# Kernel optimization log

Measured on AMD Instinct MI355X. Metric: run time of the kernel, lower is better.

## Reference

```python
import jax, jax.numpy as jnp
import numpy as np

DIM = 1024
NHEADS = 16
HEAD_DIM = DIM // NHEADS
SCALE = HEAD_DIM ** -0.5
B, N = 4, 2048


def setup_inputs() -> dict:
    key = jax.random.key(0)
    ks = jax.random.split(key, 11)
    s = 1.0 / np.sqrt(DIM)
    inp = {
        "query": jax.random.normal(ks[0], (B, N, DIM), jnp.float32),
        "key": jax.random.normal(ks[1], (B, N, DIM), jnp.float32),
        "value": jax.random.normal(ks[2], (B, N, DIM), jnp.float32),
        "Wq": jax.random.normal(ks[3], (DIM, DIM), jnp.float32) * s,
        "bq": jnp.zeros((DIM,), jnp.float32),
        "Wk": jax.random.normal(ks[4], (DIM, DIM), jnp.float32) * s,
        "bk": jnp.zeros((DIM,), jnp.float32),
        "Wv": jax.random.normal(ks[5], (DIM, DIM), jnp.float32) * s,
        "bv": jnp.zeros((DIM,), jnp.float32),
        "Wo": jax.random.normal(ks[6], (DIM, DIM), jnp.float32) * s,
        "bo": jnp.zeros((DIM,), jnp.float32),
    }
    return inp


def reference(query, key, value, Wq, bq, Wk, bk, Wv, bv, Wo, bo):
    b, n, c = query.shape
    # linear projections (torch Linear: x @ W.T + b)
    q = query @ Wq.T + bq
    k = key @ Wk.T + bk
    v = value @ Wv.T + bv
    # 'b n (h d) -> (b h) n d'
    def split_heads(t):
        return t.reshape(b, -1, NHEADS, HEAD_DIM).transpose(0, 2, 1, 3).reshape(b * NHEADS, -1, HEAD_DIM)
    q, k, v = split_heads(q), split_heads(k), split_heads(v)
    attn = jax.nn.softmax(jnp.einsum('bnd,bmd->bnm', q, k) * SCALE, axis=-1)
    # faithful to original: raw reshape [(b h), n, d] -> [b, n, c] (no head transpose back)
    x = jnp.einsum('bnm,bmd->bnd', attn, v).reshape(b, n, c)
    x = x @ Wo.T + bo
    return x
```

## Files before the change

### kernel.cpp

```cpp
#include <hip/hip_runtime.h>
#include <cstdint>
#include <cstddef>

#define NHEADS 16
#define HD 64
#define SEQ 2048
#define BATCH 4
#define DIMSZ 1024
#define MR (BATCH * SEQ)

typedef __attribute__((ext_vector_type(8))) short short8;
typedef __attribute__((ext_vector_type(4))) float f32x4;

typedef __attribute__((address_space(1))) const unsigned int as1_u32;
typedef __attribute__((address_space(3))) unsigned int as3_u32;

__device__ __forceinline__ unsigned short f2bf(float x) {
  union { float f; unsigned int u; } v; v.f = x;
  unsigned int r = v.u + 0x7FFFu + ((v.u >> 16) & 1u);
  return (unsigned short)(r >> 16);
}

__device__ __forceinline__ f32x4 mfma16(short8 a, short8 b, f32x4 c) {
  return __builtin_amdgcn_mfma_f32_16x16x32_bf16(a, b, c, 0, 0, 0);
}

__device__ __forceinline__ void gload_lds16(const void* g, void* l) {
  __builtin_amdgcn_global_load_lds((as1_u32*)g, (as3_u32*)l, 16, 0, 0);
}

__device__ __forceinline__ int swzfn(int r) { return ((r ^ (r >> 3)) & 7) << 4; }

struct Cvt7 {
  const float* s[7];
  unsigned short* d[7];
  int n4[7];
};

__global__ __launch_bounds__(256) void cvt7_k(Cvt7 a) {
  const int t = blockIdx.y;
  const float4* s = (const float4*)a.s[t];
  ushort4* d = (ushort4*)a.d[t];
  const int n4 = a.n4[t];
  for (int i = blockIdx.x * 256 + threadIdx.x; i < n4; i += gridDim.x * 256) {
    float4 f = s[i];
    ushort4 u;
    u.x = f2bf(f.x); u.y = f2bf(f.y); u.z = f2bf(f.z); u.w = f2bf(f.w);
    d[i] = u;
  }
}

struct GemmArgs {
  const unsigned short* A[3];
  const unsigned short* Bt[3];
  const float* bias[3];
  unsigned short* Cb[3];
  float* Cf[3];
  float scale[3];
  int vt[3];
};

template <bool BF16OUT>
__global__ __launch_bounds__(256) void gemm_bt_k(GemmArgs g) {
  const int z = blockIdx.z;
  const unsigned short* __restrict__ A = g.A[z];
  const unsigned short* __restrict__ Bt = g.Bt[z];
  const float* __restrict__ bias = g.bias[z];

  __shared__ unsigned short As[128 * 32];
  __shared__ unsigned short Bs[128 * 32];

  const int tid = threadIdx.x;
  const int lane = tid & 63;
  const int wave = tid >> 6;
  const int bm = blockIdx.x * 128;
  const int bn = blockIdx.y * 128;
  const int wm = (wave >> 1) * 64;
  const int wn = (wave & 1) * 64;

  const int srow = wave * 16 + (lane >> 2);
  const int scol = (lane & 3) * 8;
  const unsigned short* a_src = A + (size_t)(bm + srow) * DIMSZ + scol;
  const unsigned short* b_src = Bt + (size_t)(bn + srow) * DIMSZ + scol;
  char* a_dst = (char*)As + (size_t)(wave * 16) * 64;
  char* b_dst = (char*)Bs + (size_t)(wave * 16) * 64;

  const int fr = lane & 15;
  const int fk = (lane >> 4) * 8;

  f32x4 acc[4][4];
#pragma unroll
  for (int m = 0; m < 4; m++)
#pragma unroll
    for (int n = 0; n < 4; n++) acc[m][n] = (f32x4){0.f, 0.f, 0.f, 0.f};

  for (int k0 = 0; k0 < DIMSZ; k0 += 32) {
    __syncthreads();
    gload_lds16(a_src + k0, a_dst);
    gload_lds16(a_src + (size_t)64 * DIMSZ + k0, a_dst + 64 * 64);
    gload_lds16(b_src + k0, b_dst);
    gload_lds16(b_src + (size_t)64 * DIMSZ + k0, b_dst + 64 * 64);
    __syncthreads();

    short8 af[4], bfr[4];
#pragma unroll
    for (int m = 0; m < 4; m++) af[m] = *(const short8*)&As[(wm + m * 16 + fr) * 32 + fk];
#pragma unroll
    for (int n = 0; n < 4; n++) bfr[n] = *(const short8*)&Bs[(wn + n * 16 + fr) * 32 + fk];
#pragma unroll
    for (int m = 0; m < 4; m++)
#pragma unroll
      for (int n = 0; n < 4; n++) acc[m][n] = mfma16(af[m], bfr[n], acc[m][n]);
  }

  const int r4 = (lane >> 4) * 4;
  const float sc = g.scale[z];
  if (g.vt[z]) {
    unsigned short* vtp = g.Cb[z];
#pragma unroll
    for (int n = 0; n < 4; n++) {
      const int c = bn + wn + n * 16 + fr;
      const float bv = bias[c];
#pragma unroll
      for (int m = 0; m < 4; m++) {
        const int rr = bm + wm + m * 16 + r4;
        ushort4 u;
        u.x = f2bf((acc[m][n][0] + bv) * sc);
        u.y = f2bf((acc[m][n][1] + bv) * sc);
        u.z = f2bf((acc[m][n][2] + bv) * sc);
        u.w = f2bf((acc[m][n][3] + bv) * sc);
        const size_t idx =
            ((size_t)((rr >> 11) * NHEADS + (c >> 6)) * HD + (c & 63)) * SEQ + (rr & (SEQ - 1));
        *(ushort4*)&vtp[idx] = u;
      }
    }
  } else {
#pragma unroll
    for (int n = 0; n < 4; n++) {
      const int c = bn + wn + n * 16 + fr;
      const float bv = bias[c];
#pragma unroll
      for (int m = 0; m < 4; m++) {
#pragma unroll
        for (int j = 0; j < 4; j++) {
          const int r = bm + wm + m * 16 + r4 + j;
          const float val = (acc[m][n][j] + bv) * sc;
          if (BF16OUT)
            g.Cb[z][(size_t)r * DIMSZ + c] = f2bf(val);
          else
            g.Cf[z][(size_t)r * DIMSZ + c] = val;
        }
      }
    }
  }
}

__global__ __launch_bounds__(256) void attn_k(const unsigned short* __restrict__ q,
                                              const unsigned short* __restrict__ k,
                                              const unsigned short* __restrict__ vt,
                                              unsigned short* __restrict__ o) {
  const int tid = threadIdx.x;
  const int lane = tid & 63;
  const int wave = tid >> 6;
  const int bh = blockIdx.y;
  const int b = bh >> 4;
  const int h = bh & 15;
  const int q0 = blockIdx.x * 64;

  __shared__ unsigned short Ks[2][64 * 64];
  __shared__ unsigned short Vs[2][64 * 64];

  const int fr = lane & 15;
  const int g4 = lane >> 4;
  const int fkb = g4 * 16;

  const size_t qrow = (size_t)b * SEQ + q0 + wave * 16 + fr;
  const unsigned short* qp = q + qrow * DIMSZ + h * HD + g4 * 8;
  const short8 qa0 = *(const short8*)(qp);
  const short8 qa1 = *(const short8*)(qp + 32);

  float m_run = -1e30f, l_run = 0.f;
  f32x4 oacc[4];
#pragma unroll
  for (int n = 0; n < 4; n++) oacc[n] = (f32x4){0.f, 0.f, 0.f, 0.f};

  const size_t kvbase = (size_t)b * SEQ * DIMSZ + h * HD;
  const size_t vtbase = (size_t)bh * HD * SEQ;
  const int klrow = lane >> 3;
  const int kcb = (lane & 7) * 16;

  auto stage = [&](int t, int buf) {
    const int kv0 = t * 64;
#pragma unroll
    for (int i = 0; i < 2; i++) {
      const int row = wave * 8 + i * 32 + klrow;
      const int scol = (kcb ^ swzfn(row)) >> 1;
      gload_lds16(k + kvbase + (size_t)(kv0 + row) * DIMSZ + scol,
                  (char*)Ks[buf] + (wave * 8 + i * 32) * 128);
      gload_lds16(vt + vtbase + (size_t)row * SEQ + kv0 + scol,
                  (char*)Vs[buf] + (wave * 8 + i * 32) * 128);
    }
  };

  stage(0, 0);
  __syncthreads();
  int cur = 0;

  for (int t = 0; t < SEQ / 64; ++t) {
    if (t + 1 < SEQ / 64) stage(t + 1, cur ^ 1);

    const char* Kc = (const char*)Ks[cur];
    const char* Vc = (const char*)Vs[cur];

    f32x4 s[4];
#pragma unroll
    for (int n = 0; n < 4; n++) {
      const int row = fr + 16 * n;
      const int swz = swzfn(row);
      const short8 kb0 = *(const short8*)(Kc + ((row * 128 + fkb) ^ swz));
      const short8 kb1 = *(const short8*)(Kc + ((row * 128 + 64 + fkb) ^ swz));
      f32x4 tacc = (f32x4){0.f, 0.f, 0.f, 0.f};
      tacc = mfma16(kb0, qa0, tacc);
      tacc = mfma16(kb1, qa1, tacc);
      s[n] = tacc;
    }

    float pm = -1e30f;
#pragma unroll
    for (int n = 0; n < 4; n++)
#pragma unroll
      for (int jj = 0; jj < 4; jj++) pm = fmaxf(pm, s[n][jj]);
    pm = fmaxf(pm, __shfl_xor(pm, 16));
    pm = fmaxf(pm, __shfl_xor(pm, 32));
    const float mn = fmaxf(m_run, pm);
    const float sf = __expf(m_run - mn);
    m_run = mn;

    float pe[4][4];
    float rs = 0.f;
#pragma unroll
    for (int n = 0; n < 4; n++)
#pragma unroll
      for (int jj = 0; jj < 4; jj++) {
        const float p = __expf(s[n][jj] - mn);
        pe[n][jj] = p;
        rs += p;
      }
    rs += __shfl_xor(rs, 16);
    rs += __shfl_xor(rs, 32);
    l_run = l_run * sf + rs;

    unsigned P32[4][2];
#pragma unroll
    for (int n = 0; n < 4; n++) {
      P32[n][0] = (unsigned)f2bf(pe[n][0]) | ((unsigned)f2bf(pe[n][1]) << 16);
      P32[n][1] = (unsigned)f2bf(pe[n][2]) | ((unsigned)f2bf(pe[n][3]) << 16);
    }

    const int myn = g4 & 1;
    const int srcA = fr + 16 * ((g4 & 1) * 2 + (g4 >> 1));
    const int srcB = fr + 16 * ((g4 & 1) * 2 + ((g4 >> 1) ^ 1));
    const unsigned xA0 = myn ? P32[1][0] : P32[0][0];
    const unsigned xA1 = myn ? P32[1][1] : P32[0][1];
    const unsigned xB0 = myn ? P32[0][0] : P32[1][0];
    const unsigned xB1 = myn ? P32[0][1] : P32[1][1];
    const unsigned xC0 = myn ? P32[3][0] : P32[2][0];
    const unsigned xC1 = myn ? P32[3][1] : P32[2][1];
    const unsigned xD0 = myn ? P32[2][0] : P32[3][0];
    const unsigned xD1 = myn ? P32[2][1] : P32[3][1];
    const unsigned A0 = (unsigned)__shfl((int)xA0, srcA);
    const unsigned A1 = (unsigned)__shfl((int)xA1, srcA);
    const unsigned B0 = (unsigned)__shfl((int)xB0, srcB);
    const unsigned B1 = (unsigned)__shfl((int)xB1, srcB);
    const unsigned C0 = (unsigned)__shfl((int)xC0, srcA);
    const unsigned C1 = (unsigned)__shfl((int)xC1, srcA);
    const unsigned D0 = (unsigned)__shfl((int)xD0, srcB);
    const unsigned D1 = (unsigned)__shfl((int)xD1, srcB);

    const bool lohalf = (g4 < 2);
    union { unsigned u[4]; short8 v; } pa0, pa1;
    pa0.u[0] = lohalf ? A0 : B0;
    pa0.u[1] = lohalf ? A1 : B1;
    pa0.u[2] = lohalf ? B0 : A0;
    pa0.u[3] = lohalf ? B1 : A1;
    pa1.u[0] = lohalf ? C0 : D0;
    pa1.u[1] = lohalf ? C1 : D1;
    pa1.u[2] = lohalf ? D0 : C0;
    pa1.u[3] = lohalf ? D1 : C1;

    float sfr[4];
#pragma unroll
    for (int jj = 0; jj < 4; jj++) sfr[jj] = __shfl(sf, 20 * g4 + jj);
#pragma unroll
    for (int n = 0; n < 4; n++)
#pragma unroll
      for (int jj = 0; jj < 4; jj++) oacc[n][jj] *= sfr[jj];

#pragma unroll
    for (int n = 0; n < 4; n++) {
      const int row = fr + 16 * n;
      const int swz = swzfn(row);
      const short8 vb0 = *(const short8*)(Vc + ((row * 128 + fkb) ^ swz));
      const short8 vb1 = *(const short8*)(Vc + ((row * 128 + 64 + fkb) ^ swz));
      oacc[n] = mfma16(pa0.v, vb0, oacc[n]);
      oacc[n] = mfma16(pa1.v, vb1, oacc[n]);
    }

    __syncthreads();
    cur ^= 1;
  }

  float lr[4];
#pragma unroll
  for (int jj = 0; jj < 4; jj++) lr[jj] = __shfl(l_run, 20 * g4 + jj);
#pragma unroll
  for (int n = 0; n < 4; n++)
#pragma unroll
    for (int jj = 0; jj < 4; jj++) {
      const int row = q0 + wave * 16 + 4 * g4 + jj;
      const float val = oacc[n][jj] / lr[jj];
      o[((size_t)bh * SEQ + row) * HD + fr + 16 * n] = f2bf(val);
    }
}

extern "C" void kernel_launch(void* const* d_in, const int* in_sizes, int n_in,
                              void* d_out, int out_size, void* d_ws, size_t ws_size,
                              hipStream_t stream) {
  (void)in_sizes; (void)n_in; (void)out_size; (void)ws_size;
  const float* query = (const float*)d_in[0];
  const float* key_i = (const float*)d_in[1];
  const float* value = (const float*)d_in[2];
  const float* Wq = (const float*)d_in[3];
  const float* bq = (const float*)d_in[4];
  const float* Wk = (const float*)d_in[5];
  const float* bk = (const float*)d_in[6];
  const float* Wv = (const float*)d_in[7];
  const float* bv = (const float*)d_in[8];
  const float* Wo = (const float*)d_in[9];
  const float* bo = (const float*)d_in[10];
  float* out = (float*)d_out;

  char* ws = (char*)d_ws;
  size_t off = 0;
  auto alloc = [&](size_t bytes) -> char* {
    char* p = ws + off;
    off += (bytes + 255) & ~(size_t)255;
    return p;
  };
  const size_t big = (size_t)MR * DIMSZ * 2;
  const size_t wsz = (size_t)DIMSZ * DIMSZ * 2;
  unsigned short* xq = (unsigned short*)alloc(big);
  unsigned short* xk = (unsigned short*)alloc(big);
  unsigned short* xv = (unsigned short*)alloc(big);
  unsigned short* wqb = (unsigned short*)alloc(wsz);
  unsigned short* wkb = (unsigned short*)alloc(wsz);
  unsigned short* wvb = (unsigned short*)alloc(wsz);
  unsigned short* wob = (unsigned short*)alloc(wsz);
  unsigned short* qb = (unsigned short*)alloc(big);
  unsigned short* kb = (unsigned short*)alloc(big);
  unsigned short* vtb = (unsigned short*)alloc(big);
  unsigned short* ob = xq;

  Cvt7 ca;
  ca.s[0] = query; ca.d[0] = xq; ca.n4[0] = MR * DIMSZ / 4;
  ca.s[1] = key_i; ca.d[1] = xk; ca.n4[1] = MR * DIMSZ / 4;
  ca.s[2] = value; ca.d[2] = xv; ca.n4[2] = MR * DIMSZ / 4;
  ca.s[3] = Wq;    ca.d[3] = wqb; ca.n4[3] = DIMSZ * DIMSZ / 4;
  ca.s[4] = Wk;    ca.d[4] = wkb; ca.n4[4] = DIMSZ * DIMSZ / 4;
  ca.s[5] = Wv;    ca.d[5] = wvb; ca.n4[5] = DIMSZ * DIMSZ / 4;
  ca.s[6] = Wo;    ca.d[6] = wob; ca.n4[6] = DIMSZ * DIMSZ / 4;
  cvt7_k<<<dim3(1024, 7), 256, 0, stream>>>(ca);

  GemmArgs gp;
  gp.A[0] = xq; gp.A[1] = xk; gp.A[2] = xv;
  gp.Bt[0] = wqb; gp.Bt[1] = wkb; gp.Bt[2] = wvb;
  gp.bias[0] = bq; gp.bias[1] = bk; gp.bias[2] = bv;
  gp.Cb[0] = qb; gp.Cb[1] = kb; gp.Cb[2] = vtb;
  gp.Cf[0] = nullptr; gp.Cf[1] = nullptr; gp.Cf[2] = nullptr;
  gp.scale[0] = 0.125f; gp.scale[1] = 1.f; gp.scale[2] = 1.f;
  gp.vt[0] = 0; gp.vt[1] = 0; gp.vt[2] = 1;
  gemm_bt_k<true><<<dim3(MR / 128, DIMSZ / 128, 3), 256, 0, stream>>>(gp);

  attn_k<<<dim3(SEQ / 64, BATCH * NHEADS), 256, 0, stream>>>(qb, kb, vtb, ob);

  GemmArgs go;
  go.A[0] = ob; go.A[1] = ob; go.A[2] = ob;
  go.Bt[0] = wob; go.Bt[1] = wob; go.Bt[2] = wob;
  go.bias[0] = bo; go.bias[1] = bo; go.bias[2] = bo;
  go.Cb[0] = nullptr; go.Cb[1] = nullptr; go.Cb[2] = nullptr;
  go.Cf[0] = out; go.Cf[1] = out; go.Cf[2] = out;
  go.scale[0] = 1.f; go.scale[1] = 1.f; go.scale[2] = 1.f;
  go.vt[0] = 0; go.vt[1] = 0; go.vt[2] = 0;
  gemm_bt_k<false><<<dim3(MR / 128, DIMSZ / 128, 1), 256, 0, stream>>>(go);
}
```

Baseline: 424.1 us.

## Use 8-wave attention blocks sharing K/V tiles and drop P shuffles

Each attention block now covers 128 queries with 8 waves instead of 64 with 4, so every K/V tile staged in LDS serves twice as many query rows and each wave issues one async load per tile rather than two. The cross-lane shuffle that rearranged P into the MFMA A-operand layout is removed; V is instead read from LDS as two 4-element halves whose offsets match P's native layout. The row-sum reduction across lanes moves out of the loop to the epilogue, and swizzled LDS offsets are precomputed before the loop. In exchange there are half as many blocks, more registers per thread for the offset tables, and more 8-byte LDS reads.

Measured after the change: 391.9 us. 7.6% less time.

```diff
diff --git a/kernel.cpp b/kernel.cpp
--- a/kernel.cpp
+++ b/kernel.cpp
@@ -10,6 +10,7 @@
 #define MR (BATCH * SEQ)
 
 typedef __attribute__((ext_vector_type(8))) short short8;
+typedef __attribute__((ext_vector_type(4))) short short4v;
 typedef __attribute__((ext_vector_type(4))) float f32x4;
 
 typedef __attribute__((address_space(1))) const unsigned int as1_u32;
@@ -155,7 +156,7 @@
   }
 }
 
-__global__ __launch_bounds__(256) void attn_k(const unsigned short* __restrict__ q,
+__global__ __launch_bounds__(512) void attn_k(const unsigned short* __restrict__ q,
                                               const unsigned short* __restrict__ k,
                                               const unsigned short* __restrict__ vt,
                                               unsigned short* __restrict__ o) {
@@ -165,7 +166,7 @@
   const int bh = blockIdx.y;
   const int b = bh >> 4;
   const int h = bh & 15;
-  const int q0 = blockIdx.x * 64;
+  const int q0 = blockIdx.x * 128;
 
   __shared__ unsigned short Ks[2][64 * 64];
   __shared__ unsigned short Vs[2][64 * 64];
@@ -184,22 +185,31 @@
 #pragma unroll
   for (int n = 0; n < 4; n++) oacc[n] = (f32x4){0.f, 0.f, 0.f, 0.f};
 
-  const size_t kvbase = (size_t)b * SEQ * DIMSZ + h * HD;
-  const size_t vtbase = (size_t)bh * HD * SEQ;
+  int koff[4][2];
+  int voff[4][4];
+#pragma unroll
+  for (int n = 0; n < 4; n++) {
+    const int row = fr + 16 * n;
+    const int swz = swzfn(row);
+    koff[n][0] = (row * 128 + fkb) ^ swz;
+    koff[n][1] = (row * 128 + 64 + fkb) ^ swz;
+#pragma unroll
+    for (int c = 0; c < 4; c++) voff[n][c] = (row * 128 + (c * 32 + 8 * g4)) ^ swz;
+  }
+
   const int klrow = lane >> 3;
   const int kcb = (lane & 7) * 16;
+  const int srow = wave * 8 + klrow;
+  const int scol = (kcb ^ swzfn(srow)) >> 1;
+  const unsigned short* ksrc =
+      k + (size_t)b * SEQ * DIMSZ + h * HD + (size_t)srow * DIMSZ + scol;
+  const unsigned short* vsrc =
+      vt + (size_t)bh * HD * SEQ + (size_t)srow * SEQ + scol;
 
   auto stage = [&](int t, int buf) {
-    const int kv0 = t * 64;
-#pragma unroll
-    for (int i = 0; i < 2; i++) {
-      const int row = wave * 8 + i * 32 + klrow;
-      const int scol = (kcb ^ swzfn(row)) >> 1;
-      gload_lds16(k + kvbase + (size_t)(kv0 + row) * DIMSZ + scol,
-                  (char*)Ks[buf] + (wave * 8 + i * 32) * 128);
-      gload_lds16(vt + vtbase + (size_t)row * SEQ + kv0 + scol,
-                  (char*)Vs[buf] + (wave * 8 + i * 32) * 128);
-    }
+    const size_t kv0 = (size_t)t * 64;
+    gload_lds16(ksrc + kv0 * DIMSZ, (char*)Ks[buf] + wave * 1024);
+    gload_lds16(vsrc + kv0, (char*)Vs[buf] + wave * 1024);
   };
 
   stage(0, 0);
@@ -215,10 +225,8 @@
     f32x4 s[4];
 #pragma unroll
     for (int n = 0; n < 4; n++) {
-      const int row = fr + 16 * n;
-      const int swz = swzfn(row);
-      const short8 kb0 = *(const short8*)(Kc + ((row * 128 + fkb) ^ swz));
-      const short8 kb1 = *(const short8*)(Kc + ((row * 128 + 64 + fkb) ^ swz));
+      const short8 kb0 = *(const short8*)(Kc + koff[n][0]);
+      const short8 kb1 = *(const short8*)(Kc + koff[n][1]);
       f32x4 tacc = (f32x4){0.f, 0.f, 0.f, 0.f};
       tacc = mfma16(kb0, qa0, tacc);
       tacc = mfma16(kb1, qa1, tacc);
@@ -236,90 +244,58 @@
     const float sf = __expf(m_run - mn);
     m_run = mn;
 
-    float pe[4][4];
+    unsigned pu[4][2];
     float rs = 0.f;
 #pragma unroll
+    for (int n = 0; n < 4; n++) {
+      const float p0 = __expf(s[n][0] - mn);
+      const float p1 = __expf(s[n][1] - mn);
+      const float p2 = __expf(s[n][2] - mn);
+      const float p3 = __expf(s[n][3] - mn);
+      rs += (p0 + p1) + (p2 + p3);
+      pu[n][0] = (unsigned)f2bf(p0) | ((unsigned)f2bf(p1) << 16);
+      pu[n][1] = (unsigned)f2bf(p2) | ((unsigned)f2bf(p3) << 16);
+    }
+    l_run = l_run * sf + rs;
+
+    float sfr[4];
+#pragma unroll
+    for (int jj = 0; jj < 4; jj++) sfr[jj] = __shfl(sf, 20 * g4 + jj);
+#pragma unroll
     for (int n = 0; n < 4; n++)
 #pragma unroll
-      for (int jj = 0; jj < 4; jj++) {
-        const float p = __expf(s[n][jj] - mn);
-        pe[n][jj] = p;
-        rs += p;
-      }
-    rs += __shfl_xor(rs, 16);
-    rs += __shfl_xor(rs, 32);
-    l_run = l_run * sf + rs;
-
-    unsigned P32[4][2];
-#pragma unroll
-    for (int n = 0; n < 4; n++) {
-      P32[n][0] = (unsigned)f2bf(pe[n][0]) | ((unsigned)f2bf(pe[n][1]) << 16);
-      P32[n][1] = (unsigned)f2bf(pe[n][2]) | ((unsigned)f2bf(pe[n][3]) << 16);
-    }
-
-    const int myn = g4 & 1;
-    const int srcA = fr + 16 * ((g4 & 1) * 2 + (g4 >> 1));
-    const int srcB = fr + 16 * ((g4 & 1) * 2 + ((g4 >> 1) ^ 1));
-    const unsigned xA0 = myn ? P32[1][0] : P32[0][0];
-    const unsigned xA1 = myn ? P32[1][1] : P32[0][1];
-    const unsigned xB0 = myn ? P32[0][0] : P32[1][0];
-    const unsigned xB1 = myn ? P32[0][1] : P32[1][1];
-    const unsigned xC0 = myn ? P32[3][0] : P32[2][0];
-    const unsigned xC1 = myn ? P32[3][1] : P32[2][1];
-    const unsigned xD0 = myn ? P32[2][0] : P32[3][0];
-    const unsigned xD1 = myn ? P32[2][1] : P32[3][1];
-    const unsigned A0 = (unsigned)__shfl((int)xA0, srcA);
-    const unsigned A1 = (unsigned)__shfl((int)xA1, srcA);
-    const unsigned B0 = (unsigned)__shfl((int)xB0, srcB);
-    const unsigned B1 = (unsigned)__shfl((int)xB1, srcB);
-    const unsigned C0 = (unsigned)__shfl((int)xC0, srcA);
-    const unsigned C1 = (unsigned)__shfl((int)xC1, srcA);
-    const unsigned D0 = (unsigned)__shfl((int)xD0, srcB);
-    const unsigned D1 = (unsigned)__shfl((int)xD1, srcB);
-
-    const bool lohalf = (g4 < 2);
+      for (int jj = 0; jj < 4; jj++) oacc[n][jj] *= sfr[jj];
+
     union { unsigned u[4]; short8 v; } pa0, pa1;
-    pa0.u[0] = lohalf ? A0 : B0;
-    pa0.u[1] = lohalf ? A1 : B1;
-    pa0.u[2] = lohalf ? B0 : A0;
-    pa0.u[3] = lohalf ? B1 : A1;
-    pa1.u[0] = lohalf ? C0 : D0;
-    pa1.u[1] = lohalf ? C1 : D1;
-    pa1.u[2] = lohalf ? D0 : C0;
-    pa1.u[3] = lohalf ? D1 : C1;
-
-    float sfr[4];
-#pragma unroll
-    for (int jj = 0; jj < 4; jj++) sfr[jj] = __shfl(sf, 20 * g4 + jj);
-#pragma unroll
-    for (int n = 0; n < 4; n++)
-#pragma unroll
-      for (int jj = 0; jj < 4; jj++) oacc[n][jj] *= sfr[jj];
-
-#pragma unroll
-    for (int n = 0; n < 4; n++) {
-      const int row = fr + 16 * n;
-      const int swz = swzfn(row);
-      const short8 vb0 = *(const short8*)(Vc + ((row * 128 + fkb) ^ swz));
-      const short8 vb1 = *(const short8*)(Vc + ((row * 128 + 64 + fkb) ^ swz));
-      oacc[n] = mfma16(pa0.v, vb0, oacc[n]);
-      oacc[n] = mfma16(pa1.v, vb1, oacc[n]);
+    pa0.u[0] = pu[0][0]; pa0.u[1] = pu[0][1]; pa0.u[2] = pu[1][0]; pa0.u[3] = pu[1][1];
+    pa1.u[0] = pu[2][0]; pa1.u[1] = pu[2][1]; pa1.u[2] = pu[3][0]; pa1.u[3] = pu[3][1];
+
+#pragma unroll
+    for (int n = 0; n < 4; n++) {
+      union { short4v h[2]; short8 v; } vb0, vb1;
+      vb0.h[0] = *(const short4v*)(Vc + voff[n][0]);
+      vb0.h[1] = *(const short4v*)(Vc + voff[n][1]);
+      vb1.h[0] = *(const short4v*)(Vc + voff[n][2]);
+      vb1.h[1] = *(const short4v*)(Vc + voff[n][3]);
+      oacc[n] = mfma16(pa0.v, vb0.v, oacc[n]);
+      oacc[n] = mfma16(pa1.v, vb1.v, oacc[n]);
     }
 
     __syncthreads();
     cur ^= 1;
   }
 
-  float lr[4];
-#pragma unroll
-  for (int jj = 0; jj < 4; jj++) lr[jj] = __shfl(l_run, 20 * g4 + jj);
+  l_run += __shfl_xor(l_run, 16);
+  l_run += __shfl_xor(l_run, 32);
+  float inv[4];
+#pragma unroll
+  for (int jj = 0; jj < 4; jj++) inv[jj] = 1.f / __shfl(l_run, 20 * g4 + jj);
 #pragma unroll
   for (int n = 0; n < 4; n++)
 #pragma unroll
     for (int jj = 0; jj < 4; jj++) {
       const int row = q0 + wave * 16 + 4 * g4 + jj;
-      const float val = oacc[n][jj] / lr[jj];
-      o[((size_t)bh * SEQ + row) * HD + fr + 16 * n] = f2bf(val);
+      o[((size_t)bh * SEQ + row) * HD + fr + 16 * n] = f2bf(oacc[n][jj] * inv[jj]);
     }
 }
 
@@ -381,7 +357,7 @@
   gp.vt[0] = 0; gp.vt[1] = 0; gp.vt[2] = 1;
   gemm_bt_k<true><<<dim3(MR / 128, DIMSZ / 128, 3), 256, 0, stream>>>(gp);
 
-  attn_k<<<dim3(SEQ / 64, BATCH * NHEADS), 256, 0, stream>>>(qb, kb, vtb, ob);
+  attn_k<<<dim3(SEQ / 128, BATCH * NHEADS), 512, 0, stream>>>(qb, kb, vtb, ob);
 
   GemmArgs go;
   go.A[0] = ob; go.A[1] = ob; go.A[2] = ob;
```
